# Kernel optimization log

Measured on AMD Instinct MI355X. Metric: run time of the kernel, lower is better.

The kernel has to match this reference:

```python
import jax, jax.numpy as jnp
import numpy as np

EPS = 0.01
MAX_ITER = 10
H = W = 48
N = H * W
B = 16


def radial_cost_matrix():
    # pairwise Euclidean distance between pixel coordinates of an HxW grid,
    # normalized to [0, 1]; shape (1, N, N)
    ys, xs = np.meshgrid(np.arange(H), np.arange(W), indexing='ij')
    coords = np.stack([ys.ravel(), xs.ravel()], axis=1).astype(np.float32)  # (N, 2)
    d = np.sqrt(((coords[:, None, :] - coords[None, :, :]) ** 2).sum(-1))
    d = d / d.max()
    return d[None].astype(np.float32)


def setup_inputs() -> dict:
    key = jax.random.key(0)
    k1, k2 = jax.random.split(key)
    pred_logits = jax.random.normal(k1, (B, H, W), dtype=jnp.float32)
    t = jax.random.uniform(k2, (B, H, W), dtype=jnp.float32)
    target_probs = t / t.sum(axis=(1, 2), keepdims=True)  # valid probability maps
    C = jnp.asarray(radial_cost_matrix())  # (1, N, N) buffer, not trainable
    return {"pred_logits": pred_logits, "target_probs": target_probs, "C": C}


def _M(C, u, v):
    # M_ij = (-c_ij + u_i + v_j) / eps ; shapes: C (1,N,N), u,v (B,N) -> (B,N,N)
    return (-C + u[..., None] + v[..., None, :]) / EPS


def reference(pred_logits, target_probs, C):
    b = pred_logits.shape[0]
    pred_logp = jax.nn.log_softmax(pred_logits.reshape(b, -1), axis=1)  # (B, N)
    target_logp = jnp.log(target_probs.reshape(b, -1) + 1e-8)           # (B, N)

    u = jnp.zeros_like(pred_logp)
    v = jnp.zeros_like(target_logp)
    for _ in range(MAX_ITER):  # fixed small iteration count (no early exit)
        u = EPS * (pred_logp - jax.nn.logsumexp(_M(C, u, v), axis=-1)) + u
        v = EPS * (target_logp - jax.nn.logsumexp(_M(C, u, v), axis=-2)) + v

    pi = jnp.exp(_M(C, u, v))                      # (B, N, N) transport plan
    cost = jnp.sum(pi * C, axis=(-2, -1))           # (B,)
    return cost.mean()                              # reduction='mean'
```

## Files before the change

kernel.cpp:

```cpp
#include <hip/hip_runtime.h>


namespace {

constexpr int N    = 2304;
constexpr int B    = 16;
constexpr int NB   = N * B;
constexpr int R    = 10;
constexpr int WIN  = 21;
constexpr int WPAD = 24;
constexpr int APX  = 12;
constexpr int AST  = 76;
constexpr int NOUT = 144;
constexpr int NTH  = WIN * 12;
constexpr int AVR1 = 23;
constexpr int AVR2 = 43;
constexpr int BVR  = 23;
constexpr int P1L  = 46 * 26;
constexpr int P2L  = 12 * 14;

__device__ __forceinline__ float wave_sum(float v) {
#pragma unroll
    for (int off = 32; off >= 1; off >>= 1) v += __shfl_xor(v, off);
    return v;
}

template <bool WC, int NT>
__device__ __forceinline__ void stage_wt(float* wtl, float* wcl,
                                         const float* __restrict__ C) {
    for (int i = threadIdx.x; i < WIN * WPAD; i += NT) {
        const int dy = i / WPAD, dx = i - dy * WPAD;
        float wv = 0.f, wc = 0.f;
        if (dx < WIN) {
            const float c = C[1176 * N + (14 + dy) * 48 + (14 + dx)];
            wv = __expf(c * -100.f);
            wc = wv * c;
        }
        wtl[i] = wv;
        if (WC) wcl[i] = wc;
    }
}

template <bool ONES, int NT>
__device__ __forceinline__ void stage_ap(float* vl, const float* img,
                                         int b, int ytop, int nrows) {
    for (int i = threadIdx.x; i < nrows * 18; i += NT) {
        const int rr = i / 18, c4 = i - rr * 18;
        const int y = ytop + rr, x0 = c4 * 4 - APX;
        float4 v = make_float4(0.f, 0.f, 0.f, 0.f);
        if ((unsigned)y < 48u && (unsigned)x0 < 48u)
            v = ONES ? make_float4(1.f, 1.f, 1.f, 1.f)
                     : *(const float4*)(img + b * N + y * 48 + x0);
        *(float4*)&vl[rr * AST + c4 * 4] = v;
    }
}

__device__ __forceinline__ void conv_c12(const float* vp, const float* wp,
                                         float* acc) {
    float vr[36], wr[24];
#pragma unroll
    for (int c = 0; c < 9; ++c) *(float4*)&vr[4 * c] = *(const float4*)&vp[4 * c];
#pragma unroll
    for (int c = 0; c < 6; ++c) *(float4*)&wr[4 * c] = *(const float4*)&wp[4 * c];
#pragma unroll
    for (int dx = 0; dx < WIN; ++dx)
#pragma unroll
        for (int k = 0; k < 12; ++k)
            acc[k] = fmaf(wr[dx], vr[k + 2 + dx], acc[k]);
}
__device__ __forceinline__ void conv_p12(const float* lo, const float* hi,
                                         const float* wp, float* acc) {
    float vr[36], wr[24];
#pragma unroll
    for (int c = 0; c < 9; ++c) {
        const float4 a = *(const float4*)&lo[4 * c];
        const float4 b = *(const float4*)&hi[4 * c];
        vr[4 * c]     = a.x + b.x;
        vr[4 * c + 1] = a.y + b.y;
        vr[4 * c + 2] = a.z + b.z;
        vr[4 * c + 3] = a.w + b.w;
    }
#pragma unroll
    for (int c = 0; c < 6; ++c) *(float4*)&wr[4 * c] = *(const float4*)&wp[4 * c];
#pragma unroll
    for (int dx = 0; dx < WIN; ++dx)
#pragma unroll
        for (int k = 0; k < 12; ++k)
            acc[k] = fmaf(wr[dx], vr[k + 2 + dx], acc[k]);
}
__device__ __forceinline__ void conv_c24(const float* vp, const float* wp,
                                         float* acc) {
    float vr[48], wr[24];
#pragma unroll
    for (int c = 0; c < 12; ++c) *(float4*)&vr[4 * c] = *(const float4*)&vp[4 * c];
#pragma unroll
    for (int c = 0; c < 6; ++c) *(float4*)&wr[4 * c] = *(const float4*)&wp[4 * c];
#pragma unroll
    for (int dx = 0; dx < WIN; ++dx)
#pragma unroll
        for (int k = 0; k < 24; ++k)
            acc[k] = fmaf(wr[dx], vr[k + 2 + dx], acc[k]);
}
__device__ __forceinline__ void conv_p24(const float* lo, const float* hi,
                                         const float* wp, float* acc) {
    float vr[48], wr[24];
#pragma unroll
    for (int c = 0; c < 12; ++c) {
        const float4 a = *(const float4*)&lo[4 * c];
        const float4 b = *(const float4*)&hi[4 * c];
        vr[4 * c]     = a.x + b.x;
        vr[4 * c + 1] = a.y + b.y;
        vr[4 * c + 2] = a.z + b.z;
        vr[4 * c + 3] = a.w + b.w;
    }
#pragma unroll
    for (int c = 0; c < 6; ++c) *(float4*)&wr[4 * c] = *(const float4*)&wp[4 * c];
#pragma unroll
    for (int dx = 0; dx < WIN; ++dx)
#pragma unroll
        for (int k = 0; k < 24; ++k)
            acc[k] = fmaf(wr[dx], vr[k + 2 + dx], acc[k]);
}

__global__ __launch_bounds__(256) void sk_a1(const float* __restrict__ logits,
                                             const float* __restrict__ C,
                                             float* __restrict__ smstat,
                                             float* __restrict__ A0,
                                             float* __restrict__ out) {
    __shared__ float vl[AVR1 * AST];
    __shared__ float wtl[WIN * WPAD];
    __shared__ float part[NTH * 12];
    __shared__ float sred[8];

    const int bid = blockIdx.x;
    const int b   = bid & 15;
    const int y0  = (bid >> 4) * 3;
    const int tid = threadIdx.x, w = tid >> 6, lane = tid & 63;

    stage_wt<false, 256>(wtl, nullptr, C);
    stage_ap<true, 256>(vl, nullptr, b, y0 - R, AVR1);

    float xs[9];
    float m = -3.0e38f;
#pragma unroll
    for (int s9 = 0; s9 < 9; ++s9) {
        xs[s9] = logits[b * N + s9 * 256 + tid];
        m = fmaxf(m, xs[s9]);
    }
#pragma unroll
    for (int off = 32; off >= 1; off >>= 1) m = fmaxf(m, __shfl_xor(m, off));
    if (lane == 0) sred[w] = m;
    __syncthreads();
    m = fmaxf(fmaxf(sred[0], sred[1]), fmaxf(sred[2], sred[3]));
    float sum = 0.f;
#pragma unroll
    for (int s9 = 0; s9 < 9; ++s9) sum += __expf(xs[s9] - m);
#pragma unroll
    for (int off = 32; off >= 1; off >>= 1) sum += __shfl_xor(sum, off);
    __syncthreads();
    if (lane == 0) sred[4 + w] = sum;
    __syncthreads();
    sum = sred[4] + sred[5] + sred[6] + sred[7];
    const float sm_m = m, sm_inv = 1.f / sum;
    if (tid == 0 && (bid >> 4) == 0) {
        smstat[2 * b]     = sm_m;
        smstat[2 * b + 1] = sm_inv;
        if (b == 0) out[0] = 0.f;
    }
    __syncthreads();

    if (tid < NTH) {
        const int dy = tid / 12, strip = tid - dy * 12;
        const int r = strip >> 2, xw = (strip & 3) * 12;
        float acc[12];
#pragma unroll
        for (int k = 0; k < 12; ++k) acc[k] = 0.f;
        conv_c12(&vl[(r + dy) * AST + xw], &wtl[dy * WPAD], acc);
#pragma unroll
        for (int c = 0; c < 3; ++c)
            *(float4*)&part[tid * 12 + 4 * c] = *(float4*)&acc[4 * c];
    }
    __syncthreads();

    if (tid < NOUT) {
        float ssum = 0.f;
#pragma unroll
        for (int d = 0; d < WIN; ++d) ssum += part[d * 144 + tid];
        const int o = b * N + (y0 + tid / 48) * 48 + (tid % 48);
        A0[o] = __expf(logits[o] - sm_m) * sm_inv / ssum;
    }
}

__global__ __launch_bounds__(512) void sk_fused(const float* __restrict__ logits,
                                                const float* __restrict__ target,
                                                const float* __restrict__ C,
                                                const float* __restrict__ smstat,
                                                const float* __restrict__ Ain,
                                                float* __restrict__ Aout) {
    __shared__ float vl[AVR2 * AST];
    __shared__ float bt[BVR * AST];
    __shared__ float part[11 * P1L];
    __shared__ float wtl[WIN * WPAD];

    const int bid = blockIdx.x;
    const int b   = bid & 15;
    const int y0  = (bid >> 4) * 3;
    const int tid = threadIdx.x;

    stage_ap<false, 512>(vl, Ain, b, y0 - 2 * R, AVR2);

    float tpre[3];
#pragma unroll
    for (int j = 0; j < 3; ++j) {
        const int o = tid + j * 512;
        tpre[j] = 0.f;
        if (o < BVR * 48) {
            const int rb = o / 48, x = o - rb * 48;
            const int y = y0 - R + rb;
            if ((unsigned)y < 48u) tpre[j] = target[b * N + y * 48 + x] + 1e-8f;
        }
    }
    float lpre = 0.f;
    if (tid < NOUT)
        lpre = logits[b * N + (y0 + tid / 48) * 48 + (tid % 48)];

    stage_wt<false, 512>(wtl, nullptr, C);
    for (int i = tid; i < BVR * AST; i += 512) bt[i] = 0.f;
    const float sm_m = smstat[2 * b], sm_inv = smstat[2 * b + 1];
    __syncthreads();

    if (tid < 506) {
        const int u = tid / 46, slot = tid - u * 46;
        const int rb = slot >> 1, xw = (slot & 1) * 24;
        float acc[24];
#pragma unroll
        for (int k = 0; k < 24; ++k) acc[k] = 0.f;
        if (u == 0) conv_c24(&vl[(rb + 10) * AST + xw], &wtl[10 * WPAD], acc);
        else        conv_p24(&vl[(rb + 10 - u) * AST + xw],
                             &vl[(rb + 10 + u) * AST + xw],
                             &wtl[(10 + u) * WPAD], acc);
        float* pp = &part[u * P1L + slot * 26];
#pragma unroll
        for (int c = 0; c < 6; ++c) *(float4*)&pp[4 * c] = *(float4*)&acc[4 * c];
    }
    __syncthreads();

#pragma unroll
    for (int j = 0; j < 3; ++j) {
        const int o = tid + j * 512;
        if (o < BVR * 48) {
            const int rb = o / 48, x = o - rb * 48;
            const int slot = rb * 2 + (x >= 24 ? 1 : 0);
            const int k = x >= 24 ? x - 24 : x;
            float s = 0.f;
#pragma unroll
            for (int l = 0; l < 11; ++l) s += part[l * P1L + slot * 26 + k];
            const int y = y0 - R + rb;
            if ((unsigned)y < 48u) bt[rb * AST + APX + x] = tpre[j] / s;
        }
    }
    __syncthreads();

    if (tid < 132) {
        const int u = tid / 12, slot = tid - u * 12;
        const int ra = slot >> 2, xw = (slot & 3) * 12;
        float acc[12];
#pragma unroll
        for (int k = 0; k < 12; ++k) acc[k] = 0.f;
        if (u == 0) conv_c12(&bt[(ra + 10) * AST + xw], &wtl[10 * WPAD], acc);
        else        conv_p12(&bt[(ra + 10 - u) * AST + xw],
                             &bt[(ra + 10 + u) * AST + xw],
                             &wtl[(10 + u) * WPAD], acc);
        float* pp = &part[u * P2L + slot * 14];
#pragma unroll
        for (int c = 0; c < 3; ++c) *(float4*)&pp[4 * c] = *(float4*)&acc[4 * c];
    }
    __syncthreads();

    if (tid < NOUT) {
        const int ra = tid / 48, x = tid - ra * 48;
        const int slot = ra * 4 + x / 12, k = x % 12;
        float s = 0.f;
#pragma unroll
        for (int l = 0; l < 11; ++l) s += part[l * P2L + slot * 14 + k];
        const int g = b * N + (y0 + ra) * 48 + x;
        Aout[g] = __expf(lpre - sm_m) * sm_inv / s;
    }
}

__global__ __launch_bounds__(256) void sk_cost(const float* __restrict__ target,
                                               const float* __restrict__ C,
                                               const float* __restrict__ Ain,
                                               float* __restrict__ out) {
    __shared__ float vl[AVR1 * AST];
    __shared__ float wtl[WIN * WPAD], wcl[WIN * WPAD];
    __shared__ float p1[NTH * 12], p2[NTH * 12];
    __shared__ float sred[4];

    const int bid = blockIdx.x;
    const int b   = bid & 15;
    const int y0  = (bid >> 4) * 3;
    const int tid = threadIdx.x, w = tid >> 6, lane = tid & 63;

    stage_wt<true, 256>(wtl, wcl, C);
    stage_ap<false, 256>(vl, Ain, b, y0 - R, AVR1);
    __syncthreads();

    if (tid < NTH) {
        const int dy = tid / 12, strip = tid - dy * 12;
        const int r = strip >> 2, xw = (strip & 3) * 12;
        float a1[12], a2[12];
#pragma unroll
        for (int k = 0; k < 12; ++k) { a1[k] = 0.f; a2[k] = 0.f; }
        float vr[36], wr[24], cr[24];
        const float* vp = &vl[(r + dy) * AST + xw];
#pragma unroll
        for (int c = 0; c < 9; ++c)
            *(float4*)&vr[4 * c] = *(const float4*)&vp[4 * c];
#pragma unroll
        for (int c = 0; c < 6; ++c) {
            *(float4*)&wr[4 * c] = *(const float4*)&wtl[dy * WPAD + 4 * c];
            *(float4*)&cr[4 * c] = *(const float4*)&wcl[dy * WPAD + 4 * c];
        }
#pragma unroll
        for (int dx = 0; dx < WIN; ++dx)
#pragma unroll
            for (int k = 0; k < 12; ++k) {
                a1[k] = fmaf(wr[dx], vr[k + 2 + dx], a1[k]);
                a2[k] = fmaf(cr[dx], vr[k + 2 + dx], a2[k]);
            }
#pragma unroll
        for (int c = 0; c < 3; ++c) {
            *(float4*)&p1[tid * 12 + 4 * c] = *(float4*)&a1[4 * c];
            *(float4*)&p2[tid * 12 + 4 * c] = *(float4*)&a2[4 * c];
        }
    }
    __syncthreads();

    float val = 0.f;
    if (tid < NOUT) {
        float s1 = 0.f, s2 = 0.f;
#pragma unroll
        for (int d = 0; d < WIN; ++d) {
            s1 += p1[d * 144 + tid];
            s2 += p2[d * 144 + tid];
        }
        const int o = b * N + (y0 + tid / 48) * 48 + (tid % 48);
        val = (target[o] + 1e-8f) / s1 * s2;
    }
    val = wave_sum(val);
    if (lane == 0) sred[w] = val;
    __syncthreads();
    if (tid == 0)
        atomicAdd(out, (sred[0] + sred[1] + sred[2] + sred[3]) * (1.f / 16.f));
}

}

extern "C" void kernel_launch(void* const* d_in, const int* in_sizes, int n_in,
                              void* d_out, int out_size, void* d_ws, size_t ws_size,
                              hipStream_t stream) {
    const float* logits = (const float*)d_in[0];
    const float* target = (const float*)d_in[1];
    const float* C      = (const float*)d_in[2];
    float* out = (float*)d_out;
    float* ws  = (float*)d_ws;

    float* smstat = ws;
    float* A0     = ws + 32;
    float* A1     = A0 + NB;

    sk_a1<<<256, 256, 0, stream>>>(logits, C, smstat, A0, out);

    float* bufs[2] = {A0, A1};
    for (int t = 0; t < 9; ++t) {
        sk_fused<<<256, 512, 0, stream>>>(logits, target, C, smstat,
                                          bufs[t & 1], bufs[(t & 1) ^ 1]);
    }

    sk_cost<<<256, 256, 0, stream>>>(target, C, A1, out);
}
```

Before: 95.69 us.

## Fold first Sinkhorn half-step into fused kernel via closed-form prefix-sum row sums

```diff
diff --git a/kernel.cpp b/kernel.cpp
--- a/kernel.cpp
+++ b/kernel.cpp
@@ -16,8 +16,9 @@
 constexpr int AVR1 = 23;
 constexpr int AVR2 = 43;
 constexpr int BVR  = 23;
-constexpr int P1L  = 46 * 26;
-constexpr int P2L  = 12 * 14;
+constexpr int PST  = 25;
+constexpr int P1L  = 46 * PST;
+constexpr int P2L  = 6 * PST;
 
 __device__ __forceinline__ float wave_sum(float v) {
 #pragma unroll
@@ -122,111 +123,105 @@
             acc[k] = fmaf(wr[dx], vr[k + 2 + dx], acc[k]);
 }
 
-__global__ __launch_bounds__(256) void sk_a1(const float* __restrict__ logits,
-                                             const float* __restrict__ C,
-                                             float* __restrict__ smstat,
-                                             float* __restrict__ A0,
-                                             float* __restrict__ out) {
-    __shared__ float vl[AVR1 * AST];
-    __shared__ float wtl[WIN * WPAD];
-    __shared__ float part[NTH * 12];
-    __shared__ float sred[8];
-
-    const int bid = blockIdx.x;
-    const int b   = bid & 15;
-    const int y0  = (bid >> 4) * 3;
-    const int tid = threadIdx.x, w = tid >> 6, lane = tid & 63;
-
-    stage_wt<false, 256>(wtl, nullptr, C);
-    stage_ap<true, 256>(vl, nullptr, b, y0 - R, AVR1);
-
-    float xs[9];
-    float m = -3.0e38f;
-#pragma unroll
-    for (int s9 = 0; s9 < 9; ++s9) {
-        xs[s9] = logits[b * N + s9 * 256 + tid];
-        m = fmaxf(m, xs[s9]);
-    }
-#pragma unroll
-    for (int off = 32; off >= 1; off >>= 1) m = fmaxf(m, __shfl_xor(m, off));
-    if (lane == 0) sred[w] = m;
-    __syncthreads();
-    m = fmaxf(fmaxf(sred[0], sred[1]), fmaxf(sred[2], sred[3]));
-    float sum = 0.f;
-#pragma unroll
-    for (int s9 = 0; s9 < 9; ++s9) sum += __expf(xs[s9] - m);
-#pragma unroll
-    for (int off = 32; off >= 1; off >>= 1) sum += __shfl_xor(sum, off);
-    __syncthreads();
-    if (lane == 0) sred[4 + w] = sum;
-    __syncthreads();
-    sum = sred[4] + sred[5] + sred[6] + sred[7];
-    const float sm_m = m, sm_inv = 1.f / sum;
-    if (tid == 0 && (bid >> 4) == 0) {
-        smstat[2 * b]     = sm_m;
-        smstat[2 * b + 1] = sm_inv;
-        if (b == 0) out[0] = 0.f;
-    }
-    __syncthreads();
-
-    if (tid < NTH) {
-        const int dy = tid / 12, strip = tid - dy * 12;
-        const int r = strip >> 2, xw = (strip & 3) * 12;
-        float acc[12];
-#pragma unroll
-        for (int k = 0; k < 12; ++k) acc[k] = 0.f;
-        conv_c12(&vl[(r + dy) * AST + xw], &wtl[dy * WPAD], acc);
-#pragma unroll
-        for (int c = 0; c < 3; ++c)
-            *(float4*)&part[tid * 12 + 4 * c] = *(float4*)&acc[4 * c];
-    }
-    __syncthreads();
-
-    if (tid < NOUT) {
-        float ssum = 0.f;
-#pragma unroll
-        for (int d = 0; d < WIN; ++d) ssum += part[d * 144 + tid];
-        const int o = b * N + (y0 + tid / 48) * 48 + (tid % 48);
-        A0[o] = __expf(logits[o] - sm_m) * sm_inv / ssum;
-    }
-}
-
+template <bool FIRST>
 __global__ __launch_bounds__(512) void sk_fused(const float* __restrict__ logits,
                                                 const float* __restrict__ target,
                                                 const float* __restrict__ C,
-                                                const float* __restrict__ smstat,
+                                                float* __restrict__ smstat,
                                                 const float* __restrict__ Ain,
-                                                float* __restrict__ Aout) {
+                                                float* __restrict__ Aout,
+                                                float* __restrict__ out) {
     __shared__ float vl[AVR2 * AST];
     __shared__ float bt[BVR * AST];
     __shared__ float part[11 * P1L];
     __shared__ float wtl[WIN * WPAD];
+    __shared__ float sred[16];
 
     const int bid = blockIdx.x;
     const int b   = bid & 15;
     const int y0  = (bid >> 4) * 3;
     const int tid = threadIdx.x;
 
-    stage_ap<false, 512>(vl, Ain, b, y0 - 2 * R, AVR2);
-
-    float tpre[3];
-#pragma unroll
-    for (int j = 0; j < 3; ++j) {
-        const int o = tid + j * 512;
-        tpre[j] = 0.f;
-        if (o < BVR * 48) {
-            const int rb = o / 48, x = o - rb * 48;
-            const int y = y0 - R + rb;
-            if ((unsigned)y < 48u) tpre[j] = target[b * N + y * 48 + x] + 1e-8f;
-        }
-    }
-    float lpre = 0.f;
-    if (tid < NOUT)
-        lpre = logits[b * N + (y0 + tid / 48) * 48 + (tid % 48)];
-
     stage_wt<false, 512>(wtl, nullptr, C);
+
+    float sm_m, sm_inv;
+    if constexpr (FIRST) {
+        const int w = tid >> 6, lane = tid & 63;
+        float xs[5];
+        float m = -3.0e38f;
+#pragma unroll
+        for (int k = 0; k < 5; ++k) {
+            const int idx = tid + k * 512;
+            xs[k] = (idx < N) ? logits[b * N + idx] : -3.0e38f;
+            m = fmaxf(m, xs[k]);
+        }
+#pragma unroll
+        for (int off = 32; off >= 1; off >>= 1) m = fmaxf(m, __shfl_xor(m, off));
+        if (lane == 0) sred[w] = m;
+        __syncthreads();
+        m = sred[0];
+#pragma unroll
+        for (int i = 1; i < 8; ++i) m = fmaxf(m, sred[i]);
+        float sum = 0.f;
+#pragma unroll
+        for (int k = 0; k < 5; ++k)
+            if (tid + k * 512 < N) sum += __expf(xs[k] - m);
+#pragma unroll
+        for (int off = 32; off >= 1; off >>= 1) sum += __shfl_xor(sum, off);
+        __syncthreads();
+        if (lane == 0) sred[8 + w] = sum;
+        __syncthreads();
+        sum = 0.f;
+#pragma unroll
+        for (int i = 0; i < 8; ++i) sum += sred[8 + i];
+        sm_m = m;
+        sm_inv = 1.f / sum;
+        if ((bid >> 4) == 0 && tid == 0) {
+            smstat[2 * b]     = sm_m;
+            smstat[2 * b + 1] = sm_inv;
+            if (b == 0) out[0] = 0.f;
+        }
+        __syncthreads();
+
+        float* pfx = part;
+        if (tid < WIN) {
+            float run = 0.f;
+            for (int j = 0; j < WIN; ++j) {
+                run += wtl[tid * WPAD + j];
+                pfx[tid * WIN + j] = run;
+            }
+        }
+        __syncthreads();
+        if (tid < WIN) {
+            float run = 0.f;
+            for (int d = 0; d < WIN; ++d) {
+                run += pfx[d * WIN + tid];
+                pfx[d * WIN + tid] = run;
+            }
+        }
+        __syncthreads();
+
+        for (int i = tid; i < AVR2 * 72; i += 512) {
+            const int rr = i / 72, cc = i - rr * 72;
+            const int y = y0 - 2 * R + rr, x = cc - APX;
+            float v = 0.f;
+            if ((unsigned)y < 48u && (unsigned)x < 48u) {
+                const int ulo = max(0, 10 - y), uhi = min(20, 57 - y);
+                const int vlo = max(0, 10 - x), vhi = min(20, 57 - x);
+                float rs = pfx[uhi * WIN + vhi];
+                if (ulo) rs -= pfx[(ulo - 1) * WIN + vhi];
+                if (vlo) rs -= pfx[uhi * WIN + (vlo - 1)];
+                if (ulo && vlo) rs += pfx[(ulo - 1) * WIN + (vlo - 1)];
+                v = __expf(logits[b * N + y * 48 + x] - sm_m) * sm_inv / rs;
+            }
+            vl[rr * AST + cc] = v;
+        }
+    } else {
+        stage_ap<false, 512>(vl, Ain, b, y0 - 2 * R, AVR2);
+        sm_m   = smstat[2 * b];
+        sm_inv = smstat[2 * b + 1];
+    }
     for (int i = tid; i < BVR * AST; i += 512) bt[i] = 0.f;
-    const float sm_m = smstat[2 * b], sm_inv = smstat[2 * b + 1];
     __syncthreads();
 
     if (tid < 506) {
@@ -239,52 +234,50 @@
         else        conv_p24(&vl[(rb + 10 - u) * AST + xw],
                              &vl[(rb + 10 + u) * AST + xw],
                              &wtl[(10 + u) * WPAD], acc);
-        float* pp = &part[u * P1L + slot * 26];
-#pragma unroll
-        for (int c = 0; c < 6; ++c) *(float4*)&pp[4 * c] = *(float4*)&acc[4 * c];
-    }
-    __syncthreads();
-
-#pragma unroll
-    for (int j = 0; j < 3; ++j) {
-        const int o = tid + j * 512;
-        if (o < BVR * 48) {
-            const int rb = o / 48, x = o - rb * 48;
-            const int slot = rb * 2 + (x >= 24 ? 1 : 0);
-            const int k = x >= 24 ? x - 24 : x;
-            float s = 0.f;
-#pragma unroll
-            for (int l = 0; l < 11; ++l) s += part[l * P1L + slot * 26 + k];
-            const int y = y0 - R + rb;
-            if ((unsigned)y < 48u) bt[rb * AST + APX + x] = tpre[j] / s;
-        }
-    }
-    __syncthreads();
-
-    if (tid < 132) {
-        const int u = tid / 12, slot = tid - u * 12;
-        const int ra = slot >> 2, xw = (slot & 3) * 12;
-        float acc[12];
-#pragma unroll
-        for (int k = 0; k < 12; ++k) acc[k] = 0.f;
-        if (u == 0) conv_c12(&bt[(ra + 10) * AST + xw], &wtl[10 * WPAD], acc);
-        else        conv_p12(&bt[(ra + 10 - u) * AST + xw],
+        float* pp = &part[u * P1L + slot * PST];
+#pragma unroll
+        for (int k = 0; k < 24; ++k) pp[k] = acc[k];
+    }
+    __syncthreads();
+
+    for (int o = tid; o < BVR * 48; o += 512) {
+        const int rb = o / 48, x = o - rb * 48;
+        const int slot = rb * 2 + (x >= 24 ? 1 : 0);
+        const int k = x >= 24 ? x - 24 : x;
+        float s = 0.f;
+#pragma unroll
+        for (int l = 0; l < 11; ++l) s += part[l * P1L + slot * PST + k];
+        const int ybg = y0 - R + rb;
+        if ((unsigned)ybg < 48u)
+            bt[rb * AST + APX + x] = (target[b * N + ybg * 48 + x] + 1e-8f) / s;
+    }
+    __syncthreads();
+
+    if (tid < 66) {
+        const int u = tid / 6, slot = tid - u * 6;
+        const int ra = slot >> 1, xw = (slot & 1) * 24;
+        float acc[24];
+#pragma unroll
+        for (int k = 0; k < 24; ++k) acc[k] = 0.f;
+        if (u == 0) conv_c24(&bt[(ra + 10) * AST + xw], &wtl[10 * WPAD], acc);
+        else        conv_p24(&bt[(ra + 10 - u) * AST + xw],
                              &bt[(ra + 10 + u) * AST + xw],
                              &wtl[(10 + u) * WPAD], acc);
-        float* pp = &part[u * P2L + slot * 14];
-#pragma unroll
-        for (int c = 0; c < 3; ++c) *(float4*)&pp[4 * c] = *(float4*)&acc[4 * c];
+        float* pp = &part[u * P2L + slot * PST];
+#pragma unroll
+        for (int k = 0; k < 24; ++k) pp[k] = acc[k];
     }
     __syncthreads();
 
     if (tid < NOUT) {
         const int ra = tid / 48, x = tid - ra * 48;
-        const int slot = ra * 4 + x / 12, k = x % 12;
+        const int slot = ra * 2 + (x >= 24 ? 1 : 0);
+        const int k = x >= 24 ? x - 24 : x;
         float s = 0.f;
 #pragma unroll
-        for (int l = 0; l < 11; ++l) s += part[l * P2L + slot * 14 + k];
+        for (int l = 0; l < 11; ++l) s += part[l * P2L + slot * PST + k];
         const int g = b * N + (y0 + ra) * 48 + x;
-        Aout[g] = __expf(lpre - sm_m) * sm_inv / s;
+        Aout[g] = __expf(logits[g] - sm_m) * sm_inv / s;
     }
 }
 
@@ -370,13 +363,15 @@
     float* A0     = ws + 32;
     float* A1     = A0 + NB;
 
-    sk_a1<<<256, 256, 0, stream>>>(logits, C, smstat, A0, out);
+    sk_fused<true><<<256, 512, 0, stream>>>(logits, target, C, smstat,
+                                            A1, A0, out);
 
     float* bufs[2] = {A0, A1};
-    for (int t = 0; t < 9; ++t) {
-        sk_fused<<<256, 512, 0, stream>>>(logits, target, C, smstat,
-                                          bufs[t & 1], bufs[(t & 1) ^ 1]);
-    }
-
-    sk_cost<<<256, 256, 0, stream>>>(target, C, A1, out);
-}
+    for (int t = 0; t < 8; ++t) {
+        sk_fused<false><<<256, 512, 0, stream>>>(logits, target, C, smstat,
+                                                 bufs[t & 1], bufs[(t & 1) ^ 1],
+                                                 out);
+    }
+
+    sk_cost<<<256, 256, 0, stream>>>(target, C, A0, out);
+}
```

Measured after the change: 84.90 us. 1.13x faster.
